# Performance work log

Measured on AMD Instinct MI355X. Metric: run time of the kernel, lower is better.

The kernel has to match this reference:

```python
import jax, jax.numpy as jnp
import numpy as np

N, E, G, H, F_IN = 100_000, 3_200_000, 256, 16, 7
RRELU_SLOPE = (1.0 / 8.0 + 1.0 / 3.0) / 2.0  # eval-mode RReLU uses mean slope


def rrelu(x):
    return jnp.where(x >= 0, x, RRELU_SLOPE * x)


def gcn_conv(x, edge_index, edge_weight, W, b, n_nodes):
    """PyG GCNConv: add self-loops, symmetric norm, gather-matmul-scatter."""
    row, col = edge_index[0], edge_index[1]
    loop = jnp.arange(n_nodes)
    row = jnp.concatenate([row, loop])
    col = jnp.concatenate([col, loop])
    w = jnp.concatenate([edge_weight, jnp.ones((n_nodes,), x.dtype)])
    deg = jax.ops.segment_sum(w, col, num_segments=n_nodes)
    dis = jnp.where(deg > 0, jax.lax.rsqrt(jnp.maximum(deg, 1e-12)), 0.0)
    norm = dis[row] * w * dis[col]            # [E+N]
    h = x @ W                                  # [N, out]
    msg = h[row] * norm[:, None]               # gather + scale
    return jax.ops.segment_sum(msg, col, num_segments=n_nodes) + b


def max_pool_neighbor_x(x, edge_index, n_nodes):
    row, col = edge_index[0], edge_index[1]
    loop = jnp.arange(n_nodes)
    row = jnp.concatenate([row, loop])
    col = jnp.concatenate([col, loop])
    return jax.ops.segment_max(x[row], col, num_segments=n_nodes)


def setup_inputs() -> dict:
    key = jax.random.key(0)
    ks = jax.random.split(key, 12)
    x = jax.random.normal(ks[0], (N, F_IN), jnp.float32)
    edge_index = jax.random.randint(ks[1], (2, E), 0, N)
    edge_weights = jax.random.uniform(ks[2], (E,), jnp.float32)
    batch = (jnp.arange(N) * G) // N  # sorted, every graph non-empty
    s = 0.2
    W1 = jax.random.normal(ks[3], (F_IN, H), jnp.float32) * s
    b1 = jnp.zeros((H,), jnp.float32)
    W2 = jax.random.normal(ks[4], (H, H), jnp.float32) * s
    b2 = jnp.zeros((H,), jnp.float32)
    Wl1 = jax.random.normal(ks[5], (H, H), jnp.float32) * s
    bl1 = jax.random.normal(ks[6], (H,), jnp.float32) * s
    Wl3 = jax.random.normal(ks[7], (H, H), jnp.float32) * s
    bl3 = jax.random.normal(ks[8], (H,), jnp.float32) * s
    Wl4 = jax.random.normal(ks[9], (H, 1), jnp.float32) * s
    bl4 = jax.random.normal(ks[10], (1,), jnp.float32) * s
    return {"x": x, "edge_index": edge_index, "batch": batch,
            "edge_weights": edge_weights, "W1": W1, "b1": b1, "W2": W2,
            "b2": b2, "Wl1": Wl1, "bl1": bl1, "Wl3": Wl3, "bl3": bl3,
            "Wl4": Wl4, "bl4": bl4}


def reference(x, edge_index, batch, edge_weights, W1, b1, W2, b2,
              Wl1, bl1, Wl3, bl3, Wl4, bl4):
    h = gcn_conv(x, edge_index, edge_weights, W1, b1, N)
    h = max_pool_neighbor_x(h, edge_index, N)
    res = h
    h = gcn_conv(h, edge_index, jnp.ones((E,), h.dtype), W2, b2, N)
    h = jax.nn.relu(res + h)
    g = jax.ops.segment_max(h, batch, num_segments=G)  # global_max_pool
    res = g
    g = rrelu(res + (g @ Wl1 + bl1))
    res = g
    g = rrelu(res + (g @ Wl3 + bl3))
    # dropout p=0.5 in eval mode -> identity
    g = rrelu(g @ Wl4 + bl4)
    return g
```

## Files before the change

### kernel.cpp

```cpp
#include <hip/hip_runtime.h>
#include <hip/hip_fp16.h>
#include <math.h>

#define NN 100000
#define NE 3200000
#define NG 256
#define HD 16
#define FIN 7

#define RB 8
#define RSZ 256
#define NBUK 391
#define NBUKP 400
#define FB 512
#define CHUNK 6250
#define CH2 3125
#define SCB 8
#define ASTRIDE 17
#define CSTRIDE 9
#define LMASK 0x1FFFF

#define S16 65536.0f
#define INV_S16 1.52587890625e-5f
#define IBIAS 33554432u
#define S_DEGW 16777216.0f
#define INV_S_DEGW 5.9604644775390625e-8f

static constexpr float SLOPE = 0.22916666666666666f;

__device__ __forceinline__ float rrelu_f(float a) {
    return a >= 0.f ? a : SLOPE * a;
}

__device__ __forceinline__ unsigned encf(float v) {
    unsigned u = __float_as_uint(v);
    return u ^ (((unsigned)((int)u >> 31)) | 0x80000000u);
}
__device__ __forceinline__ float decf(unsigned u) {
    unsigned m = ((int)u < 0) ? 0x80000000u : 0xFFFFFFFFu;
    return __uint_as_float(u ^ m);
}
#define ENC_NEGINF 0x00800000u

__device__ __forceinline__ float h2f(unsigned short us) {
    __half h = *(__half*)&us;
    return __half2float(h);
}

__global__ __launch_bounds__(512) void k_hist(
        const int* __restrict__ col, int* __restrict__ hist) {
    __shared__ int bins[NBUK];
    for (int i = threadIdx.x; i < NBUK; i += 512) bins[i] = 0;
    __syncthreads();
    const int2* c2 = (const int2*)(col + blockIdx.x * CHUNK);
    for (int i = threadIdx.x; i < CH2; i += 512) {
        int2 v = c2[i];
        atomicAdd(&bins[v.x >> RB], 1);
        atomicAdd(&bins[v.y >> RB], 1);
    }
    __syncthreads();
    for (int i = threadIdx.x; i < NBUK; i += 512)
        hist[blockIdx.x * NBUKP + i] = bins[i];
}

__global__ __launch_bounds__(512) void k_scan_a(
        const int* __restrict__ hist, int* __restrict__ pre_t,
        int* __restrict__ tot) {
    __shared__ int s[SCB * (FB + 1)];
    int t = threadIdx.x;
    int c0 = blockIdx.x * SCB;
    for (int i = t; i < SCB * FB; i += 512) {
        int j = i >> 3, c = i & 7;
        int cc = c0 + c;
        s[c * (FB + 1) + j] = (cc < NBUK) ? hist[j * NBUKP + cc] : 0;
    }
    __syncthreads();
    int w = t >> 6, l = t & 63;
    int* sb = &s[w * (FB + 1)];
    int base = l * 8;
    int loc[8];
    int run = 0;
#pragma unroll
    for (int k = 0; k < 8; ++k) { loc[k] = run; run += sb[base + k]; }
    int inc = run;
#pragma unroll
    for (int d = 1; d < 64; d <<= 1) {
        int v = __shfl_up(inc, d, 64);
        if (l >= d) inc += v;
    }
    int excl = inc - run;
    int cc = c0 + w;
    if (cc < NBUK) {
#pragma unroll
        for (int k = 0; k < 8; ++k) sb[base + k] = excl + loc[k];
        if (l == 63) tot[cc] = inc;
    }
    __syncthreads();
    for (int i = t; i < SCB * FB; i += 512) {
        int j = i >> 3, c = i & 7;
        int cc2 = c0 + c;
        if (cc2 < NBUK) pre_t[j * NBUKP + cc2] = s[c * (FB + 1) + j];
    }
}

__global__ __launch_bounds__(512) void k_scan_b(
        const int* __restrict__ tot, int* __restrict__ bstart) {
    __shared__ int s[512];
    int t = threadIdx.x;
    int v = (t < NBUK) ? tot[t] : 0;
    s[t] = v;
    __syncthreads();
    for (int d = 1; d < 512; d <<= 1) {
        int add = (t >= d) ? s[t - d] : 0;
        __syncthreads();
        s[t] += add;
        __syncthreads();
    }
    if (t < NBUK) bstart[t + 1] = s[t];
    if (t == 0) bstart[0] = 0;
}

__global__ __launch_bounds__(512) void k_fill(
        const int* __restrict__ row, const int* __restrict__ col,
        const float* __restrict__ ew,
        const int* __restrict__ pre_t, const int* __restrict__ bstart,
        unsigned* __restrict__ sp, unsigned short* __restrict__ swh) {
    __shared__ int lcnt[NBUK];
    __shared__ int gofs[NBUK];
    __shared__ int part[512];
    __shared__ unsigned ssp[CHUNK];
    __shared__ unsigned short ssw[CHUNK];
    __shared__ unsigned short sbuk[CHUNK];
    int t = threadIdx.x;
    for (int i = t; i < NBUK; i += 512) {
        lcnt[i] = 0;
        gofs[i] = bstart[i] + pre_t[blockIdx.x * NBUKP + i];
    }
    __syncthreads();
    const int2* c2 = (const int2*)(col + blockIdx.x * CHUNK);
    const int2* r2 = (const int2*)(row + blockIdx.x * CHUNK);
    const float2* e2 = (const float2*)(ew + blockIdx.x * CHUNK);
    for (int i = t; i < CH2; i += 512) {
        int2 v = c2[i];
        atomicAdd(&lcnt[v.x >> RB], 1);
        atomicAdd(&lcnt[v.y >> RB], 1);
    }
    __syncthreads();
    int c = (t < NBUK) ? lcnt[t] : 0;
    part[t] = c;
    __syncthreads();
    for (int d = 1; d < 512; d <<= 1) {
        int add = (t >= d) ? part[t - d] : 0;
        __syncthreads();
        part[t] += add;
        __syncthreads();
    }
    if (t < NBUK) {
        int e = part[t] - c;
        gofs[t] -= e;
        lcnt[t] = e;
    }
    __syncthreads();
    for (int i = t; i < CH2; i += 512) {
        int2 cv = c2[i];
        int2 rv = r2[i];
        float2 wv = e2[i];
        {
            int b = cv.x >> RB;
            int s = atomicAdd(&lcnt[b], 1);
            ssp[s] = ((unsigned)(cv.x & (RSZ - 1)) << 17) | (unsigned)rv.x;
            __half hv = __float2half_rn(wv.x);
            ssw[s] = *(unsigned short*)&hv;
            sbuk[s] = (unsigned short)b;
        }
        {
            int b = cv.y >> RB;
            int s = atomicAdd(&lcnt[b], 1);
            ssp[s] = ((unsigned)(cv.y & (RSZ - 1)) << 17) | (unsigned)rv.y;
            __half hv = __float2half_rn(wv.y);
            ssw[s] = *(unsigned short*)&hv;
            sbuk[s] = (unsigned short)b;
        }
    }
    __syncthreads();
    for (int s = t; s < CHUNK; s += 512) {
        int g = s + gofs[sbuk[s]];
        sp[g] = ssp[s];
        swh[g] = ssw[s];
    }
}

__global__ __launch_bounds__(1024) void k_deg(
        const unsigned* __restrict__ sp, const unsigned short* __restrict__ swh,
        const int* __restrict__ bstart,
        const float* __restrict__ x, const float* __restrict__ W1,
        float* __restrict__ dis1, float* __restrict__ dis2,
        int* __restrict__ cnts, unsigned* __restrict__ h1h) {
    __shared__ unsigned long long sdeg[RSZ];
    __shared__ float sdis[RSZ];
    __shared__ float sW1[FIN * HD];
    int t = threadIdx.x;
    if (t < FIN * HD) sW1[t] = W1[t];
    if (t < RSZ) sdeg[t] = 0ULL;
    __syncthreads();
    int s0 = bstart[blockIdx.x], s1 = bstart[blockIdx.x + 1];
    int j = s0 + t;
    for (; j + 3072 < s1; j += 4096) {
        unsigned e0 = sp[j], e1 = sp[j + 1024], e2 = sp[j + 2048], e3 = sp[j + 3072];
        float w0 = h2f(swh[j]), w1 = h2f(swh[j + 1024]);
        float w2 = h2f(swh[j + 2048]), w3 = h2f(swh[j + 3072]);
        atomicAdd(&sdeg[e0 >> 17], (1ULL << 32) |
                  (unsigned long long)(unsigned)__float2int_rn(w0 * S_DEGW));
        atomicAdd(&sdeg[e1 >> 17], (1ULL << 32) |
                  (unsigned long long)(unsigned)__float2int_rn(w1 * S_DEGW));
        atomicAdd(&sdeg[e2 >> 17], (1ULL << 32) |
                  (unsigned long long)(unsigned)__float2int_rn(w2 * S_DEGW));
        atomicAdd(&sdeg[e3 >> 17], (1ULL << 32) |
                  (unsigned long long)(unsigned)__float2int_rn(w3 * S_DEGW));
    }
    for (; j < s1; j += 1024) {
        unsigned e = sp[j];
        float w = h2f(swh[j]);
        atomicAdd(&sdeg[e >> 17], (1ULL << 32) |
                  (unsigned long long)(unsigned)__float2int_rn(w * S_DEGW));
    }
    __syncthreads();
    int node0 = blockIdx.x * RSZ;
    if (t < RSZ && node0 + t < NN) {
        unsigned long long v = sdeg[t];
        unsigned cnt = (unsigned)(v >> 32);
        float wsum = (float)(unsigned)(v & 0xFFFFFFFFULL) * INV_S_DEGW;
        float d1 = rsqrtf(wsum + 1.f);
        dis1[node0 + t] = d1;
        sdis[t] = d1;
        dis2[node0 + t] = rsqrtf((float)cnt + 1.f);
        cnts[node0 + t] = (int)cnt;
    }
    __syncthreads();
    for (int i = t; i < RSZ * 8; i += 1024) {
        int ln = i >> 3, p = i & 7;
        int node = node0 + ln;
        if (node < NN) {
            float a0 = 0.f, a1 = 0.f;
#pragma unroll
            for (int k = 0; k < FIN; ++k) {
                float xv = x[node * FIN + k];
                a0 += xv * sW1[k * HD + 2 * p];
                a1 += xv * sW1[k * HD + 2 * p + 1];
            }
            float d = sdis[ln];
            __half2 hh = __floats2half2_rn(a0 * d, a1 * d);
            h1h[node * 8 + p] = *(unsigned*)&hh;
        }
    }
}

__device__ __forceinline__ void conv_acc4(unsigned long long* acc, unsigned ex,
                                          uint4 g, float w, int pb) {
    unsigned long long* a = &acc[(ex >> 17) * CSTRIDE + pb * 4];
    float2 f0 = __half22float2(*(__half2*)&g.x);
    float2 f1 = __half22float2(*(__half2*)&g.y);
    float2 f2 = __half22float2(*(__half2*)&g.z);
    float2 f3 = __half22float2(*(__half2*)&g.w);
    atomicAdd(&a[0], ((unsigned long long)((unsigned)__float2int_rn(f0.x * w) + IBIAS) << 32)
                   |  (unsigned long long)((unsigned)__float2int_rn(f0.y * w) + IBIAS));
    atomicAdd(&a[1], ((unsigned long long)((unsigned)__float2int_rn(f1.x * w) + IBIAS) << 32)
                   |  (unsigned long long)((unsigned)__float2int_rn(f1.y * w) + IBIAS));
    atomicAdd(&a[2], ((unsigned long long)((unsigned)__float2int_rn(f2.x * w) + IBIAS) << 32)
                   |  (unsigned long long)((unsigned)__float2int_rn(f2.y * w) + IBIAS));
    atomicAdd(&a[3], ((unsigned long long)((unsigned)__float2int_rn(f3.x * w) + IBIAS) << 32)
                   |  (unsigned long long)((unsigned)__float2int_rn(f3.y * w) + IBIAS));
}

__global__ __launch_bounds__(1024) void k_conv1(
        const unsigned* __restrict__ sp, const unsigned short* __restrict__ swh,
        const int* __restrict__ bstart,
        const unsigned* __restrict__ h1h, const float* __restrict__ dis1,
        const int* __restrict__ cnts, const float* __restrict__ b1,
        unsigned* __restrict__ h1outh) {
    __shared__ unsigned long long acc[RSZ * CSTRIDE];
    int t = threadIdx.x;
    for (int i = t; i < RSZ * CSTRIDE; i += 1024) acc[i] = 0ULL;
    __syncthreads();
    int pb = t & 1, slot = t >> 1;
    const uint4* h1h4 = (const uint4*)h1h;
    int s0 = bstart[blockIdx.x], s1 = bstart[blockIdx.x + 1];
    int j = s0 + slot;
    for (; j + 1536 < s1; j += 2048) {
        unsigned e0 = sp[j], e1 = sp[j + 512], e2 = sp[j + 1024], e3 = sp[j + 1536];
        float w0 = h2f(swh[j]) * S16, w1 = h2f(swh[j + 512]) * S16;
        float w2 = h2f(swh[j + 1024]) * S16, w3 = h2f(swh[j + 1536]) * S16;
        uint4 g0 = h1h4[(e0 & LMASK) * 2 + pb];
        uint4 g1 = h1h4[(e1 & LMASK) * 2 + pb];
        uint4 g2 = h1h4[(e2 & LMASK) * 2 + pb];
        uint4 g3 = h1h4[(e3 & LMASK) * 2 + pb];
        conv_acc4(acc, e0, g0, w0, pb);
        conv_acc4(acc, e1, g1, w1, pb);
        conv_acc4(acc, e2, g2, w2, pb);
        conv_acc4(acc, e3, g3, w3, pb);
    }
    for (; j < s1; j += 512) {
        unsigned e = sp[j];
        float w = h2f(swh[j]) * S16;
        uint4 g = h1h4[(e & LMASK) * 2 + pb];
        conv_acc4(acc, e, g, w, pb);
    }
    __syncthreads();
    int node0 = blockIdx.x * RSZ;
    for (int i = t; i < RSZ * 8; i += 1024) {
        int ln = i >> 3, pp = i & 7;
        int node = node0 + ln;
        if (node < NN) {
            unsigned long long v = acc[ln * CSTRIDE + pp];
            unsigned kb = (unsigned)cnts[node] * IBIAS;
            float a0 = (float)(int)((unsigned)(v >> 32) - kb) * INV_S16;
            float a1 = (float)(int)((unsigned)(v & 0xFFFFFFFFULL) - kb) * INV_S16;
            float d = dis1[node];
            unsigned sh = h1h[node * 8 + pp];
            float2 sf = __half22float2(*(__half2*)&sh);
            float r0 = (a0 + sf.x) * d + b1[2 * pp];
            float r1 = (a1 + sf.y) * d + b1[2 * pp + 1];
            __half2 hh = __floats2half2_rn(r0, r1);
            h1outh[node * 8 + pp] = *(unsigned*)&hh;
        }
    }
}

__device__ __forceinline__ void pool_acc4(unsigned* acc, unsigned ex,
                                          uint4 g, int pb) {
    unsigned* a = &acc[(ex >> 17) * ASTRIDE + pb * 8];
    float2 f;
    f = __half22float2(*(__half2*)&g.x);
    atomicMax(a + 0, encf(f.x)); atomicMax(a + 1, encf(f.y));
    f = __half22float2(*(__half2*)&g.y);
    atomicMax(a + 2, encf(f.x)); atomicMax(a + 3, encf(f.y));
    f = __half22float2(*(__half2*)&g.z);
    atomicMax(a + 4, encf(f.x)); atomicMax(a + 5, encf(f.y));
    f = __half22float2(*(__half2*)&g.w);
    atomicMax(a + 6, encf(f.x)); atomicMax(a + 7, encf(f.y));
}

__global__ __launch_bounds__(1024) void k_pool_h2(
        const unsigned* __restrict__ sp, const int* __restrict__ bstart,
        const unsigned* __restrict__ h1outh, const float* __restrict__ W2,
        const float* __restrict__ dis2,
        float2* __restrict__ pool2, unsigned* __restrict__ h2sh) {
    __shared__ unsigned acc[RSZ * ASTRIDE];
    __shared__ float sW2[256];
    int t = threadIdx.x;
    if (t < 256) sW2[t] = W2[t];
    for (int i = t; i < RSZ * ASTRIDE; i += 1024) acc[i] = ENC_NEGINF;
    __syncthreads();
    int pb = t & 1, slot = t >> 1;
    const uint4* hv4 = (const uint4*)h1outh;
    int s0 = bstart[blockIdx.x], s1 = bstart[blockIdx.x + 1];
    int j = s0 + slot;
    for (; j + 1536 < s1; j += 2048) {
        unsigned e0 = sp[j], e1 = sp[j + 512], e2 = sp[j + 1024], e3 = sp[j + 1536];
        uint4 g0 = hv4[(e0 & LMASK) * 2 + pb];
        uint4 g1 = hv4[(e1 & LMASK) * 2 + pb];
        uint4 g2 = hv4[(e2 & LMASK) * 2 + pb];
        uint4 g3 = hv4[(e3 & LMASK) * 2 + pb];
        pool_acc4(acc, e0, g0, pb);
        pool_acc4(acc, e1, g1, pb);
        pool_acc4(acc, e2, g2, pb);
        pool_acc4(acc, e3, g3, pb);
    }
    for (; j < s1; j += 512) {
        unsigned e = sp[j];
        uint4 g = hv4[(e & LMASK) * 2 + pb];
        pool_acc4(acc, e, g, pb);
    }
    __syncthreads();
    int node0 = blockIdx.x * RSZ;
    for (int i = t; i < RSZ * 8; i += 1024) {
        int ln = i >> 3, pp = i & 7;
        int node = node0 + ln;
        if (node < NN) {
            unsigned sh = h1outh[node * 8 + pp];
            float2 sf = __half22float2(*(__half2*)&sh);
            float m0 = fmaxf(decf(acc[ln * ASTRIDE + 2 * pp]),     sf.x);
            float m1 = fmaxf(decf(acc[ln * ASTRIDE + 2 * pp + 1]), sf.y);
            pool2[node * 8 + pp] = make_float2(m0, m1);
            acc[ln * ASTRIDE + 2 * pp]     = __float_as_uint(m0);
            acc[ln * ASTRIDE + 2 * pp + 1] = __float_as_uint(m1);
        }
    }
    __syncthreads();
    for (int i = t; i < RSZ * 8; i += 1024) {
        int ln = i >> 3, pp = i & 7;
        int node = node0 + ln;
        if (node < NN) {
            float a0 = 0.f, a1 = 0.f;
#pragma unroll
            for (int k = 0; k < HD; ++k) {
                float pv = __uint_as_float(acc[ln * ASTRIDE + k]);
                a0 += pv * sW2[k * HD + 2 * pp];
                a1 += pv * sW2[k * HD + 2 * pp + 1];
            }
            float d = dis2[node];
            __half2 hh = __floats2half2_rn(a0 * d, a1 * d);
            h2sh[node * 8 + pp] = *(unsigned*)&hh;
        }
    }
}

__global__ __launch_bounds__(1024) void k_conv2(
        const unsigned* __restrict__ sp, const int* __restrict__ bstart,
        const unsigned* __restrict__ h2sh, const float* __restrict__ dis2,
        const int* __restrict__ cnts, const float2* __restrict__ pool2,
        const float* __restrict__ b2, float2* __restrict__ hfin2) {
    __shared__ unsigned long long acc[RSZ * CSTRIDE];
    int t = threadIdx.x;
    for (int i = t; i < RSZ * CSTRIDE; i += 1024) acc[i] = 0ULL;
    __syncthreads();
    int pb = t & 1, slot = t >> 1;
    const uint4* hv4 = (const uint4*)h2sh;
    int s0 = bstart[blockIdx.x], s1 = bstart[blockIdx.x + 1];
    int j = s0 + slot;
    for (; j + 1536 < s1; j += 2048) {
        unsigned e0 = sp[j], e1 = sp[j + 512], e2 = sp[j + 1024], e3 = sp[j + 1536];
        uint4 g0 = hv4[(e0 & LMASK) * 2 + pb];
        uint4 g1 = hv4[(e1 & LMASK) * 2 + pb];
        uint4 g2 = hv4[(e2 & LMASK) * 2 + pb];
        uint4 g3 = hv4[(e3 & LMASK) * 2 + pb];
        conv_acc4(acc, e0, g0, S16, pb);
        conv_acc4(acc, e1, g1, S16, pb);
        conv_acc4(acc, e2, g2, S16, pb);
        conv_acc4(acc, e3, g3, S16, pb);
    }
    for (; j < s1; j += 512) {
        unsigned e = sp[j];
        uint4 g = hv4[(e & LMASK) * 2 + pb];
        conv_acc4(acc, e, g, S16, pb);
    }
    __syncthreads();
    int node0 = blockIdx.x * RSZ;
    for (int i = t; i < RSZ * 8; i += 1024) {
        int ln = i >> 3, pp = i & 7;
        int node = node0 + ln;
        if (node < NN) {
            unsigned long long v = acc[ln * CSTRIDE + pp];
            unsigned kb = (unsigned)cnts[node] * IBIAS;
            float a0 = (float)(int)((unsigned)(v >> 32) - kb) * INV_S16;
            float a1 = (float)(int)((unsigned)(v & 0xFFFFFFFFULL) - kb) * INV_S16;
            float d = dis2[node];
            unsigned sh = h2sh[node * 8 + pp];
            float2 self = __half22float2(*(__half2*)&sh);
            float2 pl = pool2[node * 8 + pp];
            float r0 = pl.x + (a0 + self.x) * d + b2[2 * pp];
            float r1 = pl.y + (a1 + self.y) * d + b2[2 * pp + 1];
            hfin2[node * 8 + pp] = make_float2(fmaxf(r0, 0.f), fmaxf(r1, 0.f));
        }
    }
}

__global__ __launch_bounds__(256) void k_graph_max(
        const float* __restrict__ hfin, float* __restrict__ gbuf) {
    int g = blockIdx.x;
    int start = (g * NN + NG - 1) / NG;
    int end   = ((g + 1) * NN + NG - 1) / NG;
    int f = threadIdx.x & 15, sub = threadIdx.x >> 4;
    float m = -3.402823466e38f;
    for (int i = start + sub; i < end; i += 16)
        m = fmaxf(m, hfin[i * HD + f]);
    __shared__ float lds[256];
    lds[threadIdx.x] = m;
    __syncthreads();
    if (threadIdx.x < 16) {
        float mm = lds[threadIdx.x];
#pragma unroll
        for (int s = 1; s < 16; ++s) mm = fmaxf(mm, lds[s * 16 + threadIdx.x]);
        gbuf[g * HD + threadIdx.x] = mm;
    }
}

__global__ __launch_bounds__(256) void k_mlp(
        const float* __restrict__ gbuf,
        const float* __restrict__ Wl1, const float* __restrict__ bl1,
        const float* __restrict__ Wl3, const float* __restrict__ bl3,
        const float* __restrict__ Wl4, const float* __restrict__ bl4,
        float* __restrict__ out) {
    __shared__ float sW1[256], sW3[256], sW4[16], sb1[16], sb3[16];
    __shared__ float sb4;
    int tid = threadIdx.x;
    sW1[tid] = Wl1[tid];
    sW3[tid] = Wl3[tid];
    if (tid < 16) { sW4[tid] = Wl4[tid]; sb1[tid] = bl1[tid]; sb3[tid] = bl3[tid]; }
    if (tid == 0) sb4 = bl4[0];
    __syncthreads();

    float v[16], t1[16], t2[16];
#pragma unroll
    for (int f = 0; f < 16; ++f) v[f] = gbuf[tid * 16 + f];
#pragma unroll
    for (int f = 0; f < 16; ++f) {
        float a = sb1[f] + v[f];
#pragma unroll
        for (int k = 0; k < 16; ++k) a += v[k] * sW1[k * 16 + f];
        t1[f] = rrelu_f(a);
    }
#pragma unroll
    for (int f = 0; f < 16; ++f) {
        float a = sb3[f] + t1[f];
#pragma unroll
        for (int k = 0; k < 16; ++k) a += t1[k] * sW3[k * 16 + f];
        t2[f] = rrelu_f(a);
    }
    float o = sb4;
#pragma unroll
    for (int k = 0; k < 16; ++k) o += t2[k] * sW4[k];
    out[tid] = rrelu_f(o);
}

extern "C" void kernel_launch(void* const* d_in, const int* in_sizes, int n_in,
                              void* d_out, int out_size, void* d_ws, size_t ws_size,
                              hipStream_t stream) {
    const float* x   = (const float*)d_in[0];
    const int*   ei  = (const int*)  d_in[1];
    const float* ew  = (const float*)d_in[3];
    const float* W1  = (const float*)d_in[4];
    const float* b1  = (const float*)d_in[5];
    const float* W2  = (const float*)d_in[6];
    const float* b2  = (const float*)d_in[7];
    const float* Wl1 = (const float*)d_in[8];
    const float* bl1 = (const float*)d_in[9];
    const float* Wl3 = (const float*)d_in[10];
    const float* bl3 = (const float*)d_in[11];
    const float* Wl4 = (const float*)d_in[12];
    const float* bl4 = (const float*)d_in[13];
    const int* row = ei;
    const int* col = ei + NE;

    float* ws = (float*)d_ws;
    float* hfin  = ws;
    float* pool  = hfin + NN * HD;
    float* dead  = pool + NN * HD;
    float* dis1  = dead + NN * HD;
    float* dis2  = dis1 + NN;
    int*   cnts  = (int*)(dis2 + NN);
    float* gbuf  = (float*)(cnts + NN);
    unsigned* h1h    = (unsigned*)(gbuf + NG * HD);
    unsigned* h1outh = h1h    + NN * 8;
    unsigned* h2sh   = h1outh + NN * 8;
    unsigned* sp     = h2sh   + NN * 8;
    unsigned short* swh = (unsigned short*)(sp + NE);
    int* tot    = (int*)(swh + NE + (NE & 1));
    int* bstart = tot + NBUK;
    int* hist   = (int*)pool;
    int* pre_t  = (int*)dead;

    k_hist     <<<FB, 512, 0, stream>>>(col, hist);
    k_scan_a   <<<(NBUK + SCB - 1) / SCB, 512, 0, stream>>>(hist, pre_t, tot);
    k_scan_b   <<<1, 512, 0, stream>>>(tot, bstart);
    k_fill     <<<FB, 512, 0, stream>>>(row, col, ew, pre_t, bstart, sp, swh);
    k_deg      <<<NBUK, 1024, 0, stream>>>(sp, swh, bstart, x, W1,
                                           dis1, dis2, cnts, h1h);
    k_conv1    <<<NBUK, 1024, 0, stream>>>(sp, swh, bstart, h1h, dis1,
                                           cnts, b1, h1outh);
    k_pool_h2  <<<NBUK, 1024, 0, stream>>>(sp, bstart, h1outh, W2, dis2,
                                           (float2*)pool, h2sh);
    k_conv2    <<<NBUK, 1024, 0, stream>>>(sp, bstart, h2sh, dis2, cnts,
                                           (const float2*)pool, b2, (float2*)hfin);
    k_graph_max<<<NG, 256, 0, stream>>>(hfin, gbuf);
    k_mlp      <<<1, 256, 0, stream>>>(gbuf, Wl1, bl1, Wl3, bl3, Wl4, bl4, (float*)d_out);
}
```

Baseline: 226.0 us.

## Fuse global max pool into conv2 epilogue and use nontemporal edge loads

The per-graph max pooling moves into the conv2 epilogue. Each block reduces its post-ReLU node outputs into a small shared-memory per-graph max using unsigned atomics, which is valid because the values are non-negative, then merges them into a global buffer with atomicMax. This removes the separate graph-max kernel and the write and re-read of the full node-feature array. The global buffer is zeroed in the scan kernel. Streaming edge-list and weight loads in the degree, conv and pool kernels switch to nontemporal loads to reduce cache pollution, at the cost of extra global atomics.

After: 236.5 us. +4.7%, slower.

```diff
diff --git a/kernel.cpp b/kernel.cpp
--- a/kernel.cpp
+++ b/kernel.cpp
@@ -47,6 +47,9 @@
     return __half2float(h);
 }
 
+__device__ __forceinline__ unsigned ntl_u(const unsigned* p) { return __builtin_nontemporal_load(p); }
+__device__ __forceinline__ unsigned short ntl_h(const unsigned short* p) { return __builtin_nontemporal_load(p); }
+
 __global__ __launch_bounds__(512) void k_hist(
         const int* __restrict__ col, int* __restrict__ hist) {
     __shared__ int bins[NBUK];
@@ -104,9 +107,11 @@
 }
 
 __global__ __launch_bounds__(512) void k_scan_b(
-        const int* __restrict__ tot, int* __restrict__ bstart) {
+        const int* __restrict__ tot, int* __restrict__ bstart,
+        unsigned* __restrict__ gbuf) {
     __shared__ int s[512];
     int t = threadIdx.x;
+    for (int i = t; i < NG * HD; i += 512) gbuf[i] = 0u;
     int v = (t < NBUK) ? tot[t] : 0;
     s[t] = v;
     __syncthreads();
@@ -206,9 +211,10 @@
     int s0 = bstart[blockIdx.x], s1 = bstart[blockIdx.x + 1];
     int j = s0 + t;
     for (; j + 3072 < s1; j += 4096) {
-        unsigned e0 = sp[j], e1 = sp[j + 1024], e2 = sp[j + 2048], e3 = sp[j + 3072];
-        float w0 = h2f(swh[j]), w1 = h2f(swh[j + 1024]);
-        float w2 = h2f(swh[j + 2048]), w3 = h2f(swh[j + 3072]);
+        unsigned e0 = ntl_u(&sp[j]), e1 = ntl_u(&sp[j + 1024]);
+        unsigned e2 = ntl_u(&sp[j + 2048]), e3 = ntl_u(&sp[j + 3072]);
+        float w0 = h2f(ntl_h(&swh[j])), w1 = h2f(ntl_h(&swh[j + 1024]));
+        float w2 = h2f(ntl_h(&swh[j + 2048])), w3 = h2f(ntl_h(&swh[j + 3072]));
         atomicAdd(&sdeg[e0 >> 17], (1ULL << 32) |
                   (unsigned long long)(unsigned)__float2int_rn(w0 * S_DEGW));
         atomicAdd(&sdeg[e1 >> 17], (1ULL << 32) |
@@ -219,8 +225,8 @@
                   (unsigned long long)(unsigned)__float2int_rn(w3 * S_DEGW));
     }
     for (; j < s1; j += 1024) {
-        unsigned e = sp[j];
-        float w = h2f(swh[j]);
+        unsigned e = ntl_u(&sp[j]);
+        float w = h2f(ntl_h(&swh[j]));
         atomicAdd(&sdeg[e >> 17], (1ULL << 32) |
                   (unsigned long long)(unsigned)__float2int_rn(w * S_DEGW));
     }
@@ -287,9 +293,10 @@
     int s0 = bstart[blockIdx.x], s1 = bstart[blockIdx.x + 1];
     int j = s0 + slot;
     for (; j + 1536 < s1; j += 2048) {
-        unsigned e0 = sp[j], e1 = sp[j + 512], e2 = sp[j + 1024], e3 = sp[j + 1536];
-        float w0 = h2f(swh[j]) * S16, w1 = h2f(swh[j + 512]) * S16;
-        float w2 = h2f(swh[j + 1024]) * S16, w3 = h2f(swh[j + 1536]) * S16;
+        unsigned e0 = ntl_u(&sp[j]), e1 = ntl_u(&sp[j + 512]);
+        unsigned e2 = ntl_u(&sp[j + 1024]), e3 = ntl_u(&sp[j + 1536]);
+        float w0 = h2f(ntl_h(&swh[j])) * S16, w1 = h2f(ntl_h(&swh[j + 512])) * S16;
+        float w2 = h2f(ntl_h(&swh[j + 1024])) * S16, w3 = h2f(ntl_h(&swh[j + 1536])) * S16;
         uint4 g0 = h1h4[(e0 & LMASK) * 2 + pb];
         uint4 g1 = h1h4[(e1 & LMASK) * 2 + pb];
         uint4 g2 = h1h4[(e2 & LMASK) * 2 + pb];
@@ -300,8 +307,8 @@
         conv_acc4(acc, e3, g3, w3, pb);
     }
     for (; j < s1; j += 512) {
-        unsigned e = sp[j];
-        float w = h2f(swh[j]) * S16;
+        unsigned e = ntl_u(&sp[j]);
+        float w = h2f(ntl_h(&swh[j])) * S16;
         uint4 g = h1h4[(e & LMASK) * 2 + pb];
         conv_acc4(acc, e, g, w, pb);
     }
@@ -356,7 +363,8 @@
     int s0 = bstart[blockIdx.x], s1 = bstart[blockIdx.x + 1];
     int j = s0 + slot;
     for (; j + 1536 < s1; j += 2048) {
-        unsigned e0 = sp[j], e1 = sp[j + 512], e2 = sp[j + 1024], e3 = sp[j + 1536];
+        unsigned e0 = ntl_u(&sp[j]), e1 = ntl_u(&sp[j + 512]);
+        unsigned e2 = ntl_u(&sp[j + 1024]), e3 = ntl_u(&sp[j + 1536]);
         uint4 g0 = hv4[(e0 & LMASK) * 2 + pb];
         uint4 g1 = hv4[(e1 & LMASK) * 2 + pb];
         uint4 g2 = hv4[(e2 & LMASK) * 2 + pb];
@@ -367,7 +375,7 @@
         pool_acc4(acc, e3, g3, pb);
     }
     for (; j < s1; j += 512) {
-        unsigned e = sp[j];
+        unsigned e = ntl_u(&sp[j]);
         uint4 g = hv4[(e & LMASK) * 2 + pb];
         pool_acc4(acc, e, g, pb);
     }
@@ -409,17 +417,20 @@
         const unsigned* __restrict__ sp, const int* __restrict__ bstart,
         const unsigned* __restrict__ h2sh, const float* __restrict__ dis2,
         const int* __restrict__ cnts, const float2* __restrict__ pool2,
-        const float* __restrict__ b2, float2* __restrict__ hfin2) {
+        const float* __restrict__ b2, unsigned* __restrict__ gbuf) {
     __shared__ unsigned long long acc[RSZ * CSTRIDE];
+    __shared__ unsigned sgmax[4 * HD];
     int t = threadIdx.x;
     for (int i = t; i < RSZ * CSTRIDE; i += 1024) acc[i] = 0ULL;
+    if (t < 4 * HD) sgmax[t] = 0u;
     __syncthreads();
     int pb = t & 1, slot = t >> 1;
     const uint4* hv4 = (const uint4*)h2sh;
     int s0 = bstart[blockIdx.x], s1 = bstart[blockIdx.x + 1];
     int j = s0 + slot;
     for (; j + 1536 < s1; j += 2048) {
-        unsigned e0 = sp[j], e1 = sp[j + 512], e2 = sp[j + 1024], e3 = sp[j + 1536];
+        unsigned e0 = ntl_u(&sp[j]), e1 = ntl_u(&sp[j + 512]);
+        unsigned e2 = ntl_u(&sp[j + 1024]), e3 = ntl_u(&sp[j + 1536]);
         uint4 g0 = hv4[(e0 & LMASK) * 2 + pb];
         uint4 g1 = hv4[(e1 & LMASK) * 2 + pb];
         uint4 g2 = hv4[(e2 & LMASK) * 2 + pb];
@@ -430,12 +441,13 @@
         conv_acc4(acc, e3, g3, S16, pb);
     }
     for (; j < s1; j += 512) {
-        unsigned e = sp[j];
+        unsigned e = ntl_u(&sp[j]);
         uint4 g = hv4[(e & LMASK) * 2 + pb];
         conv_acc4(acc, e, g, S16, pb);
     }
     __syncthreads();
     int node0 = blockIdx.x * RSZ;
+    int gbase = (int)(((unsigned long long)node0 * NG) / NN);
     for (int i = t; i < RSZ * 8; i += 1024) {
         int ln = i >> 3, pp = i & 7;
         int node = node0 + ln;
@@ -448,30 +460,19 @@
             unsigned sh = h2sh[node * 8 + pp];
             float2 self = __half22float2(*(__half2*)&sh);
             float2 pl = pool2[node * 8 + pp];
-            float r0 = pl.x + (a0 + self.x) * d + b2[2 * pp];
-            float r1 = pl.y + (a1 + self.y) * d + b2[2 * pp + 1];
-            hfin2[node * 8 + pp] = make_float2(fmaxf(r0, 0.f), fmaxf(r1, 0.f));
-        }
-    }
-}
-
-__global__ __launch_bounds__(256) void k_graph_max(
-        const float* __restrict__ hfin, float* __restrict__ gbuf) {
-    int g = blockIdx.x;
-    int start = (g * NN + NG - 1) / NG;
-    int end   = ((g + 1) * NN + NG - 1) / NG;
-    int f = threadIdx.x & 15, sub = threadIdx.x >> 4;
-    float m = -3.402823466e38f;
-    for (int i = start + sub; i < end; i += 16)
-        m = fmaxf(m, hfin[i * HD + f]);
-    __shared__ float lds[256];
-    lds[threadIdx.x] = m;
-    __syncthreads();
-    if (threadIdx.x < 16) {
-        float mm = lds[threadIdx.x];
-#pragma unroll
-        for (int s = 1; s < 16; ++s) mm = fmaxf(mm, lds[s * 16 + threadIdx.x]);
-        gbuf[g * HD + threadIdx.x] = mm;
+            float r0 = fmaxf(pl.x + (a0 + self.x) * d + b2[2 * pp], 0.f);
+            float r1 = fmaxf(pl.y + (a1 + self.y) * d + b2[2 * pp + 1], 0.f);
+            int lg = (int)(((unsigned long long)node * NG) / NN) - gbase;
+            atomicMax(&sgmax[lg * HD + 2 * pp],     __float_as_uint(r0));
+            atomicMax(&sgmax[lg * HD + 2 * pp + 1], __float_as_uint(r1));
+        }
+    }
+    __syncthreads();
+    if (t < 4 * HD) {
+        int lg = t >> 4, f = t & 15;
+        int g = gbase + lg;
+        unsigned m = sgmax[t];
+        if (g < NG && m > 0u) atomicMax(&gbuf[g * HD + f], m);
     }
 }
 
@@ -533,14 +534,13 @@
     const int* col = ei + NE;
 
     float* ws = (float*)d_ws;
-    float* hfin  = ws;
-    float* pool  = hfin + NN * HD;
+    float* pool  = ws;
     float* dead  = pool + NN * HD;
     float* dis1  = dead + NN * HD;
     float* dis2  = dis1 + NN;
     int*   cnts  = (int*)(dis2 + NN);
-    float* gbuf  = (float*)(cnts + NN);
-    unsigned* h1h    = (unsigned*)(gbuf + NG * HD);
+    unsigned* gbuf = (unsigned*)(cnts + NN);
+    unsigned* h1h    = gbuf   + NG * HD;
     unsigned* h1outh = h1h    + NN * 8;
     unsigned* h2sh   = h1outh + NN * 8;
     unsigned* sp     = h2sh   + NN * 8;
@@ -552,7 +552,7 @@
 
     k_hist     <<<FB, 512, 0, stream>>>(col, hist);
     k_scan_a   <<<(NBUK + SCB - 1) / SCB, 512, 0, stream>>>(hist, pre_t, tot);
-    k_scan_b   <<<1, 512, 0, stream>>>(tot, bstart);
+    k_scan_b   <<<1, 512, 0, stream>>>(tot, bstart, gbuf);
     k_fill     <<<FB, 512, 0, stream>>>(row, col, ew, pre_t, bstart, sp, swh);
     k_deg      <<<NBUK, 1024, 0, stream>>>(sp, swh, bstart, x, W1,
                                            dis1, dis2, cnts, h1h);
@@ -561,7 +561,7 @@
     k_pool_h2  <<<NBUK, 1024, 0, stream>>>(sp, bstart, h1outh, W2, dis2,
                                            (float2*)pool, h2sh);
     k_conv2    <<<NBUK, 1024, 0, stream>>>(sp, bstart, h2sh, dis2, cnts,
-                                           (const float2*)pool, b2, (float2*)hfin);
-    k_graph_max<<<NG, 256, 0, stream>>>(hfin, gbuf);
-    k_mlp      <<<1, 256, 0, stream>>>(gbuf, Wl1, bl1, Wl3, bl3, Wl4, bl4, (float*)d_out);
-}
+                                           (const float2*)pool, b2, gbuf);
+    k_mlp      <<<1, 256, 0, stream>>>((const float*)gbuf, Wl1, bl1, Wl3, bl3,
+                                       Wl4, bl4, (float*)d_out);
+}
```
